# Performance work log

Measured on AMD Instinct MI355X. Metric: run time of the kernel, lower is better.

Reference implementation:

```python
import jax, jax.numpy as jnp
import numpy as np

N, E, G = 20000, 320000, 256
F = 128
C = [256, 512, 1024]
NHID, NOUT = 1024, 768
EPS = 1e-5


def setup_inputs() -> dict:
    key = jax.random.key(0)
    keys = iter(jax.random.split(key, 64))
    def nrm(shape, s=0.02):
        return jax.random.normal(next(keys), shape, jnp.float32) * s
    inp = {}
    inp["x"] = jax.random.normal(next(keys), (N, F), jnp.float32)
    inp["edge_index"] = jax.random.randint(next(keys), (2, E), 0, N)
    inp["batch"] = jnp.sort(jax.random.randint(next(keys), (N,), 0, G))
    # stem GCNConv: F -> C[0]
    inp["w0"] = nrm((F, C[0])); inp["b0"] = jnp.zeros((C[0],), jnp.float32)
    # residual blocks
    for i in range(2):
        cin, cout = C[i], C[i + 1]
        mid = cin + (cout - cin) // 2
        p = f"blk{i}_"
        inp[p + "w1"] = nrm((cin, mid)); inp[p + "b1"] = jnp.zeros((mid,), jnp.float32)
        inp[p + "g1"] = jnp.ones((mid,), jnp.float32); inp[p + "be1"] = jnp.zeros((mid,), jnp.float32)
        inp[p + "w2"] = nrm((mid, cout)); inp[p + "b2"] = jnp.zeros((cout,), jnp.float32)
        inp[p + "g2"] = jnp.ones((cout,), jnp.float32); inp[p + "be2"] = jnp.zeros((cout,), jnp.float32)
        inp[p + "w3"] = nrm((cin, cout)); inp[p + "b3"] = jnp.zeros((cout,), jnp.float32)
    inp["mw1"] = nrm((C[-1], NHID)); inp["mb1"] = jnp.zeros((NHID,), jnp.float32)
    inp["mw2"] = nrm((NHID, NOUT)); inp["mb2"] = jnp.zeros((NOUT,), jnp.float32)
    return inp


def _gcn(x, w, b, src, dst, dinv):
    # PyG GCNConv: D^{-1/2}(A+I)D^{-1/2} X W + b, deg computed with self-loops
    xw = x @ w                                     # [N, Cout]
    msg = xw[src] * dinv[src, None]                # [E, Cout]
    agg = jax.ops.segment_sum(msg, dst, num_segments=x.shape[0])
    return agg * dinv[:, None] + xw * (dinv * dinv)[:, None] + b


def _bn(h, g, b):
    # BatchNorm1d in training mode: biased batch statistics over nodes
    m = h.mean(axis=0)
    v = h.var(axis=0)
    return g * (h - m) * jax.lax.rsqrt(v + EPS) + b


def reference(x, edge_index, batch, w0, b0,
              blk0_w1, blk0_b1, blk0_g1, blk0_be1, blk0_w2, blk0_b2, blk0_g2, blk0_be2, blk0_w3, blk0_b3,
              blk1_w1, blk1_b1, blk1_g1, blk1_be1, blk1_w2, blk1_b2, blk1_g2, blk1_be2, blk1_w3, blk1_b3,
              mw1, mb1, mw2, mb2):
    src, dst = edge_index[0], edge_index[1]
    deg = 1.0 + jax.ops.segment_sum(jnp.ones((src.shape[0],), x.dtype), dst, num_segments=x.shape[0])
    dinv = jax.lax.rsqrt(deg)                      # deg >= 1, no zero guard needed

    h = jax.nn.relu(_gcn(x, w0, b0, src, dst, dinv))
    blocks = [
        (blk0_w1, blk0_b1, blk0_g1, blk0_be1, blk0_w2, blk0_b2, blk0_g2, blk0_be2, blk0_w3, blk0_b3),
        (blk1_w1, blk1_b1, blk1_g1, blk1_be1, blk1_w2, blk1_b2, blk1_g2, blk1_be2, blk1_w3, blk1_b3),
    ]
    for (w1, b1, g1, be1, w2, b2, g2, be2, w3, b3) in blocks:
        t = jax.nn.relu(_bn(_gcn(h, w1, b1, src, dst, dinv), g1, be1))
        t = jax.nn.relu(_bn(_gcn(t, w2, b2, src, dst, dinv), g2, be2))
        h = jax.nn.relu(t) + _gcn(h, w3, b3, src, dst, dinv)

    # global mean pool over graphs
    s = jax.ops.segment_sum(h, batch, num_segments=G)
    cnt = jax.ops.segment_sum(jnp.ones((h.shape[0],), h.dtype), batch, num_segments=G)
    pooled = s / jnp.maximum(cnt, 1.0)[:, None]    # [G, C[-1]]

    out = jax.nn.relu(pooled @ mw1 + mb1) @ mw2 + mb2
    return out
```

## Files before the change

### kernel.cpp

```cpp
#include <hip/hip_runtime.h>
#include <cstdint>
#include <cstddef>

#define NN 20000
#define NE 320000
#define NG 256
#define NB 79

typedef unsigned short u16;
typedef __attribute__((ext_vector_type(8))) short bf16x8;
typedef __attribute__((ext_vector_type(4))) float f32x4;

__device__ inline float b2f(u16 h){
  union { unsigned u; float f; } v; v.u = ((unsigned)h) << 16; return v.f;
}
__device__ inline u16 f2b(float f){
  union { float f; unsigned u; } v; v.f = f;
  unsigned r = v.u + 0x7FFFu + ((v.u >> 16) & 1u);
  return (u16)(r >> 16);
}
__device__ inline void up8(const uint4& v, float* a){
  union { unsigned u; float f; } t;
  t.u = v.x << 16;         a[0] = t.f;
  t.u = v.x & 0xffff0000u; a[1] = t.f;
  t.u = v.y << 16;         a[2] = t.f;
  t.u = v.y & 0xffff0000u; a[3] = t.f;
  t.u = v.z << 16;         a[4] = t.f;
  t.u = v.z & 0xffff0000u; a[5] = t.f;
  t.u = v.w << 16;         a[6] = t.f;
  t.u = v.w & 0xffff0000u; a[7] = t.f;
}
__device__ inline unsigned pk2(float a, float b){
  return (unsigned)f2b(a) | (((unsigned)f2b(b)) << 16);
}

__device__ inline void gload_lds16(const void* g, void* l){
  __builtin_amdgcn_global_load_lds(
      (const __attribute__((address_space(1))) unsigned int*)g,
      (__attribute__((address_space(3))) unsigned int*)l, 16, 0, 0);
}


__global__ void k_zero(int* __restrict__ p, int n){
  int i = blockIdx.x*blockDim.x + threadIdx.x;
  if (i < n) p[i] = 0;
}

__global__ void k_deg(const int* __restrict__ ei, int* __restrict__ deg){
  int e = blockIdx.x*blockDim.x + threadIdx.x;
  if (e < NE) atomicAdd(&deg[ei[NE + e]], 1);
}

__global__ void k_scan1(const int* __restrict__ counts, int* __restrict__ bsum,
                        float* __restrict__ dinv){
  __shared__ int sm[256];
  int b = blockIdx.x, tid = threadIdx.x, idx = b*256 + tid;
  int v = (idx < NN) ? counts[idx] : 0;
  if (idx < NN) dinv[idx] = rsqrtf(1.0f + (float)v);
  sm[tid] = v;
  __syncthreads();
  for (int d = 128; d > 0; d >>= 1){
    if (tid < d) sm[tid] += sm[tid + d];
    __syncthreads();
  }
  if (tid == 0) bsum[b] = sm[0];
}
__global__ void k_scan2(int* __restrict__ bsum){
  if (threadIdx.x == 0){
    int c = 0;
    for (int i = 0; i < NB; i++){ int t = bsum[i]; bsum[i] = c; c += t; }
    bsum[NB] = c;
  }
}
__global__ void k_scan3(const int* __restrict__ counts, const int* __restrict__ bsum,
                        int* __restrict__ offs){
  __shared__ int sm[256];
  int b = blockIdx.x, tid = threadIdx.x, idx = b*256 + tid;
  int v = (idx < NN) ? counts[idx] : 0;
  sm[tid] = v;
  __syncthreads();
  for (int d = 1; d < 256; d <<= 1){
    int t = (tid >= d) ? sm[tid - d] : 0;
    __syncthreads();
    sm[tid] += t;
    __syncthreads();
  }
  if (idx < NN) offs[idx] = bsum[b] + sm[tid] - v;
  if (idx == NN - 1) offs[NN] = bsum[NB];
}

__global__ void k_fill(const int* __restrict__ ei, const int* __restrict__ offs,
                       int* __restrict__ cur, int* __restrict__ srcs){
  int e = blockIdx.x*blockDim.x + threadIdx.x;
  if (e < NE){
    int s = ei[e];
    int d = ei[NE + e];
    int p = atomicAdd(&cur[d], 1);
    srcs[offs[d] + p] = s;
  }
}

__global__ void k_bounds(const int* __restrict__ batch, int* __restrict__ start){
  int i = blockIdx.x*blockDim.x + threadIdx.x;
  if (i < NN){
    int b  = batch[i];
    int bp = (i == 0) ? -1 : batch[i-1];
    for (int g = bp + 1; g <= b; g++) start[g] = i;
    if (i == NN - 1){
      for (int g = b + 1; g <= NG; g++) start[g] = NN;
    }
  }
}

__global__ void k_cast(const float4* __restrict__ x, ushort4* __restrict__ xb,
                       const float* __restrict__ dinv, int total4){
  int t = blockIdx.x*blockDim.x + threadIdx.x;
  if (t >= total4) return;
  float di = dinv[t >> 5];
  float4 v = x[t];
  ushort4 o; o.x = f2b(v.x * di); o.y = f2b(v.y * di);
  o.z = f2b(v.z * di); o.w = f2b(v.w * di);
  xb[t] = o;
}

struct WPArgs {
  const float* w[7];
  u16* wt[7];
  int K[7], N[7];
  int tstart[8];
};
__global__ __launch_bounds__(256) void k_wprep7(WPArgs a){
  __shared__ float sm[64][65];
  int bid = blockIdx.x;
  int wi = 0;
  while (wi < 6 && bid >= a.tstart[wi+1]) wi++;
  int tt = bid - a.tstart[wi];
  int K = a.K[wi], N = a.N[wi];
  int nk = K >> 6;
  int kb = (tt % nk) * 64, nb = (tt / nk) * 64;
  const float* w = a.w[wi];
  u16* wt = a.wt[wi];
  int tid = threadIdx.x;
  #pragma unroll
  for (int i = 0; i < 16; i++){
    int t = i*256 + tid;
    int r = t >> 6, c = t & 63;
    sm[r][c] = w[(size_t)(kb + r) * N + nb + c];
  }
  __syncthreads();
  #pragma unroll
  for (int i = 0; i < 16; i++){
    int t = i*256 + tid;
    int r = t >> 6, c = t & 63;
    wt[(size_t)(nb + r) * K + kb + c] = f2b(sm[c][r]);
  }
}

template<int C8>
__global__ __launch_bounds__(256) void k_bnscale(uint4* __restrict__ buf,
                        const float* __restrict__ dinv,
                        const float* __restrict__ sumv, const float* __restrict__ sqv,
                        const float* __restrict__ gam,  const float* __restrict__ bet){
  int t = blockIdx.x*blockDim.x + threadIdx.x;
  if (t >= NN * C8) return;
  int i = t / C8;
  int c = t - i * C8;
  float sc[8], sh[8];
  #pragma unroll
  for (int k = 0; k < 8; k++){
    int ch = c*8 + k;
    float m  = sumv[ch] * (1.0f / NN);
    float vv = sqv[ch] * (1.0f / NN) - m * m;
    float rs = rsqrtf(vv + 1e-5f);
    sc[k] = gam[ch] * rs;
    sh[k] = bet[ch] - m * sc[k];
  }
  float di = dinv[i];
  float a[8];
  up8(buf[t], a);
  #pragma unroll
  for (int k = 0; k < 8; k++) a[k] = fmaxf(fmaf(a[k], sc[k], sh[k]), 0.f) * di;
  uint4 o;
  o.x = pk2(a[0], a[1]); o.y = pk2(a[2], a[3]);
  o.z = pk2(a[4], a[5]); o.w = pk2(a[6], a[7]);
  buf[t] = o;
}

template<int C8, int C8G>
__global__ __launch_bounds__(256) void k_agg_b(const uint4* __restrict__ in, uint4* __restrict__ out,
                        const float* __restrict__ dinv, const int* __restrict__ offs,
                        const int* __restrict__ srcs){
  constexpr bool PART = (C8G != C8);
  int bid = blockIdx.x;
  int g = PART ? (bid & 7) : 0;
  int t = PART ? ((bid >> 3)*256 + threadIdx.x) : (bid*256 + threadIdx.x);
  if (t >= NN * C8G) return;
  int i = t / C8G;
  int c = g * C8G + (t - i * C8G);
  float acc[8];
  up8(in[(size_t)i * C8 + c], acc);
  int e = offs[i], e1 = offs[i + 1];
  for (; e + 4 <= e1; e += 4){
    int sA = srcs[e], sB = srcs[e+1], sC = srcs[e+2], sD = srcs[e+3];
    uint4 yA = in[(size_t)sA * C8 + c];
    uint4 yB = in[(size_t)sB * C8 + c];
    uint4 yC = in[(size_t)sC * C8 + c];
    uint4 yD = in[(size_t)sD * C8 + c];
    float b[8];
    up8(yA, b);
    #pragma unroll
    for (int k = 0; k < 8; k++) acc[k] += b[k];
    up8(yB, b);
    #pragma unroll
    for (int k = 0; k < 8; k++) acc[k] += b[k];
    up8(yC, b);
    #pragma unroll
    for (int k = 0; k < 8; k++) acc[k] += b[k];
    up8(yD, b);
    #pragma unroll
    for (int k = 0; k < 8; k++) acc[k] += b[k];
  }
  for (; e < e1; e++){
    int s = srcs[e];
    float b[8];
    up8(in[(size_t)s * C8 + c], b);
    #pragma unroll
    for (int k = 0; k < 8; k++) acc[k] += b[k];
  }
  float di = dinv[i];
  #pragma unroll
  for (int k = 0; k < 8; k++) acc[k] *= di;
  uint4 o;
  o.x = pk2(acc[0], acc[1]); o.y = pk2(acc[2], acc[3]);
  o.z = pk2(acc[4], acc[5]); o.w = pk2(acc[6], acc[7]);
  out[(size_t)i * C8 + c] = o;
}

template<int MODE, bool STATS, bool SCALE>
__global__ __launch_bounds__(256, 4) void k_mfma(const u16* __restrict__ A,
                                                 const u16* __restrict__ BT,
                                                 const float* __restrict__ bias,
                                                 u16* __restrict__ C,
                                                 float* __restrict__ p0,
                                                 float* __restrict__ p1,
                                                 const float* __restrict__ p2,
                                                 const float* __restrict__ p3,
                                                 const float* __restrict__ dv,
                                                 int M, int K, int Nc){
  __shared__ u16 S[128*128];
  u16* As = S;
  u16* Bs = S + 128*64;
  const int tid = threadIdx.x;
  const int lane = tid & 63;
  const int quad = lane >> 4;
  const int l16 = lane & 15;
  const int wid = tid >> 6;
  const int wm = wid & 1, wn = wid >> 1;

  const int nwg = gridDim.x * gridDim.y;
  const int p = blockIdx.y * gridDim.x + blockIdx.x;
  const int xcd = p & 7;
  const int q = nwg >> 3, r = nwg & 7;
  const int w = (xcd < r ? xcd * (q + 1) : r * (q + 1) + (xcd - r) * q) + (p >> 3);
  const int bn = (w % gridDim.x) * 128;
  const int bm = (w / gridDim.x) * 128;

  f32x4 acc[4][4];
  #pragma unroll
  for (int i = 0; i < 4; i++)
    #pragma unroll
    for (int j = 0; j < 4; j++)
      acc[i][j] = (f32x4){0.f, 0.f, 0.f, 0.f};

  const int srow = tid >> 3;
  const int scol8 = tid & 7;
  for (int k0 = 0; k0 < K; k0 += 64){
    #pragma unroll
    for (int i = 0; i < 4; i++){
      int row = i*32 + srow;
      int gc = (scol8 ^ (row & 7)) * 8;
      int lofs = row*64 + scol8*8;
      gload_lds16(A + (size_t)(bm + row) * K + k0 + gc, As + lofs);
      gload_lds16(BT + (size_t)(bn + row) * K + k0 + gc, Bs + lofs);
    }
    __syncthreads();
    #pragma unroll
    for (int kk = 0; kk < 2; kk++){
      const int col8 = kk*4 + quad;
      bf16x8 af[4], bfr[4];
      #pragma unroll
      for (int mi = 0; mi < 4; mi++){
        int row = wm*64 + mi*16 + l16;
        af[mi] = *(const bf16x8*)(As + row*64 + ((col8 ^ (row & 7)) * 8));
      }
      #pragma unroll
      for (int ni = 0; ni < 4; ni++){
        int row = wn*64 + ni*16 + l16;
        bfr[ni] = *(const bf16x8*)(Bs + row*64 + ((col8 ^ (row & 7)) * 8));
      }
      #pragma unroll
      for (int mi = 0; mi < 4; mi++)
        #pragma unroll
        for (int ni = 0; ni < 4; ni++)
          acc[mi][ni] = __builtin_amdgcn_mfma_f32_16x16x32_bf16(af[mi], bfr[ni], acc[mi][ni], 0, 0, 0);
    }
    __syncthreads();
  }
  #pragma unroll
  for (int ni = 0; ni < 4; ni++){
    int colL = wn*64 + ni*16 + l16;
    float bb = bias[bn + colL];
    float s = 0.f, s2 = 0.f;
    #pragma unroll
    for (int mi = 0; mi < 4; mi++){
      int rbase = wm*64 + mi*16 + quad*4;
      #pragma unroll
      for (int r2 = 0; r2 < 4; r2++){
        int rowL = rbase + r2;
        float v = acc[mi][ni][r2] + bb;
        if (STATS && (bm + rowL) < M){ s += v; s2 += v * v; }
        if (MODE == 1) v = fmaxf(v, 0.f);
        S[rowL*128 + colL] = f2b(v);
      }
    }
    if (STATS){
      s  += __shfl_xor(s, 16, 64);  s  += __shfl_xor(s, 32, 64);
      s2 += __shfl_xor(s2, 16, 64); s2 += __shfl_xor(s2, 32, 64);
      if (quad == 0){
        atomicAdd(&p0[bn + colL], s);
        atomicAdd(&p1[bn + colL], s2);
      }
    }
  }
  __syncthreads();
  #pragma unroll
  for (int it = 0; it < 8; it++){
    int idx = it*256 + tid;
    int rl = idx >> 4, cq = idx & 15;
    int row = bm + rl;
    if (row < M){
      int col0 = bn + cq*8;
      uint4 wv = *(const uint4*)(S + rl*128 + cq*8);
      u16* cp = C + (size_t)row * Nc + col0;
      if (MODE == 3){
        float di = SCALE ? dv[row] : 1.f;
        float o[8], ov[8];
        up8(wv, o);
        uint4 old = *(const uint4*)cp;
        up8(old, ov);
        #pragma unroll
        for (int k = 0; k < 8; k++){
          int ch = col0 + k;
          float m  = p0[ch] * (1.0f / NN);
          float vv = p1[ch] * (1.0f / NN) - m * m;
          float rs = rsqrtf(vv + 1e-5f);
          float sc = p2[ch] * rs;
          float sh = p3[ch] - m * sc;
          o[k] += fmaxf(fmaf(ov[k], sc, sh), 0.f);
          if (SCALE) o[k] *= di;
        }
        uint4 ou;
        ou.x = pk2(o[0], o[1]); ou.y = pk2(o[2], o[3]);
        ou.z = pk2(o[4], o[5]); ou.w = pk2(o[6], o[7]);
        *(uint4*)cp = ou;
      } else if (SCALE){
        float di = dv[row];
        float o[8];
        up8(wv, o);
        #pragma unroll
        for (int k = 0; k < 8; k++) o[k] *= di;
        uint4 ou;
        ou.x = pk2(o[0], o[1]); ou.y = pk2(o[2], o[3]);
        ou.z = pk2(o[4], o[5]); ou.w = pk2(o[6], o[7]);
        *(uint4*)cp = ou;
      } else {
        *(uint4*)cp = wv;
      }
    }
  }
}

template<bool RELUA>
__global__ __launch_bounds__(256) void k_gemm_sk(const float* __restrict__ A,
                                                 const float* __restrict__ B,
                                                 const float* __restrict__ bias,
                                                 float* __restrict__ C,
                                                 int M, int K, int Nc){
  __shared__ float As[16][68];
  __shared__ float Bs[16][64];
  const int tid = threadIdx.x;
  const int tx = tid & 15, ty = tid >> 4;
  const int bm = blockIdx.x * 64, bn = blockIdx.y * 64;
  const int kchunk = K / gridDim.z;
  const int ks = blockIdx.z * kchunk, ke = ks + kchunk;
  const int arow = tid >> 2, akq = (tid & 3) << 2;
  const int brow = tid >> 4, bcol = (tid & 15) << 2;
  float acc[4][4] = {{0.f}};
  const bool aval = (bm + arow) < M;
  const float* Aptr = A + (size_t)(bm + arow) * K + akq;
  const float* Bptr = B + (size_t)brow * Nc + bn + bcol;
  for (int k0 = ks; k0 < ke; k0 += 16){
    float4 av = make_float4(0.f, 0.f, 0.f, 0.f);
    if (aval) av = *(const float4*)(Aptr + k0);
    if (RELUA){
      av.x = fmaxf(av.x, 0.f); av.y = fmaxf(av.y, 0.f);
      av.z = fmaxf(av.z, 0.f); av.w = fmaxf(av.w, 0.f);
    }
    float4 bv = *(const float4*)(Bptr + (size_t)k0 * Nc);
    As[akq + 0][arow] = av.x;
    As[akq + 1][arow] = av.y;
    As[akq + 2][arow] = av.z;
    As[akq + 3][arow] = av.w;
    *(float4*)&Bs[brow][bcol] = bv;
    __syncthreads();
    #pragma unroll
    for (int kk = 0; kk < 16; kk++){
      const float4 a = *(const float4*)(&As[kk][ty << 2]);
      const float4 b = *(const float4*)(&Bs[kk][tx << 2]);
      const float ar[4] = {a.x, a.y, a.z, a.w};
      const float br[4] = {b.x, b.y, b.z, b.w};
      #pragma unroll
      for (int i = 0; i < 4; i++)
        #pragma unroll
        for (int j = 0; j < 4; j++)
          acc[i][j] = fmaf(ar[i], br[j], acc[i][j]);
    }
    __syncthreads();
  }
  const int col = bn + (tx << 2);
  float4 bb = make_float4(0.f, 0.f, 0.f, 0.f);
  if (blockIdx.z == 0) bb = *(const float4*)(bias + col);
  #pragma unroll
  for (int i = 0; i < 4; i++){
    int row = bm + (ty << 2) + i;
    if (row < M){
      float* cp = C + (size_t)row * Nc + col;
      atomicAdd(cp + 0, acc[i][0] + bb.x);
      atomicAdd(cp + 1, acc[i][1] + bb.y);
      atomicAdd(cp + 2, acc[i][2] + bb.z);
      atomicAdd(cp + 3, acc[i][3] + bb.w);
    }
  }
}

__global__ __launch_bounds__(256) void k_pool_b(const u16* __restrict__ h,
                                                const int* __restrict__ start,
                                                float* __restrict__ pooled){
  __shared__ float sm[128*8];
  int g = blockIdx.x;
  int half = threadIdx.x >> 7;
  int cb = threadIdx.x & 127;
  int c = cb << 3;
  int r0 = start[g], r1 = start[g + 1];
  float acc[8] = {0.f,0.f,0.f,0.f,0.f,0.f,0.f,0.f};
  for (int r = r0 + half; r < r1; r += 2){
    float b[8];
    up8(*(const uint4*)(h + (size_t)r * 1024 + c), b);
    #pragma unroll
    for (int k = 0; k < 8; k++) acc[k] += b[k];
  }
  if (half){
    #pragma unroll
    for (int k = 0; k < 8; k++) sm[cb*8 + k] = acc[k];
  }
  __syncthreads();
  if (!half){
    float inv = (r1 > r0) ? (1.0f / (float)(r1 - r0)) : 0.0f;
    float o[8];
    #pragma unroll
    for (int k = 0; k < 8; k++) o[k] = (acc[k] + sm[cb*8 + k]) * inv;
    float4* dst = (float4*)(pooled + (size_t)g * 1024 + c);
    dst[0] = make_float4(o[0], o[1], o[2], o[3]);
    dst[1] = make_float4(o[4], o[5], o[6], o[7]);
  }
}


extern "C" void kernel_launch(void* const* d_in, const int* in_sizes, int n_in,
                              void* d_out, int out_size, void* d_ws, size_t ws_size,
                              hipStream_t stream) {
  const float* x    = (const float*)d_in[0];
  const int*   ei   = (const int*)d_in[1];
  const int*   bat  = (const int*)d_in[2];
  const float* w0   = (const float*)d_in[3];
  const float* b0   = (const float*)d_in[4];
  const float* a_w1 = (const float*)d_in[5],  *a_b1  = (const float*)d_in[6];
  const float* a_g1 = (const float*)d_in[7],  *a_be1 = (const float*)d_in[8];
  const float* a_w2 = (const float*)d_in[9],  *a_b2  = (const float*)d_in[10];
  const float* a_g2 = (const float*)d_in[11], *a_be2 = (const float*)d_in[12];
  const float* a_w3 = (const float*)d_in[13], *a_b3  = (const float*)d_in[14];
  const float* c_w1 = (const float*)d_in[15], *c_b1  = (const float*)d_in[16];
  const float* c_g1 = (const float*)d_in[17], *c_be1 = (const float*)d_in[18];
  const float* c_w2 = (const float*)d_in[19], *c_b2  = (const float*)d_in[20];
  const float* c_g2 = (const float*)d_in[21], *c_be2 = (const float*)d_in[22];
  const float* c_w3 = (const float*)d_in[23], *c_b3  = (const float*)d_in[24];
  const float* mw1  = (const float*)d_in[25], *mb1   = (const float*)d_in[26];
  const float* mw2  = (const float*)d_in[27], *mb2   = (const float*)d_in[28];
  float* out = (float*)d_out;

  char* pp = (char*)d_ws;
  auto alloc = [&](size_t b)->char*{ char* r = pp; pp += (b + 255) & ~(size_t)255; return r; };

  const size_t CH = (size_t)NN * 2;
  char* R = alloc(2304 * CH);
  float* dinv = (float*)alloc((size_t)NN * 4);
  int* icomb  = (int*)alloc((size_t)2 * NN * 4);
  int* deg    = icomb;
  int* cur    = icomb + NN;
  int* offs   = (int*)alloc((size_t)(NN + 1) * 4);
  int* bsum   = (int*)alloc((size_t)(NB + 1) * 4);
  int* srcs   = (int*)alloc((size_t)NE * 4);
  int* startg = (int*)alloc((size_t)(NG + 1) * 4);
  float* SB   = (float*)alloc(5376 * 4);
  float* sA1 = SB;
  float* sA2 = SB + 768;
  float* sC1 = SB + 1792;
  float* sC2 = SB + 3328;
  u16* WT  = (u16*)alloc(2162688 * 2);
  u16* wt0  = WT;
  u16* wtA1 = WT + 32768;
  u16* wtA2 = WT + 131072;
  u16* wtA3 = WT + 327680;
  u16* wtC1 = WT + 458752;
  u16* wtC2 = WT + 851968;
  u16* wtC3 = WT + 1638400;
  float* P  = (float*)WT;
  float* Hh = P + (size_t)NG * 1024;

  auto slot = [&](int s)->u16*{ return (u16*)(R + (size_t)s * CH); };
  u16* xb  = slot(512);
  u16* ax  = slot(0);
  u16* h0  = slot(128);
  u16* ah0 = slot(1664);
  u16* t1  = slot(1920);
  u16* at  = slot(1280);
  u16* h1  = slot(768);
  u16* ah1 = slot(1792);
  u16* u1  = slot(0);
  u16* au  = slot(1024);
  u16* h2  = slot(0);

  auto cdiv = [](int a, int b){ return (a + b - 1) / b; };

  k_zero<<<cdiv(2*NN,256),256,0,stream>>>(icomb, 2*NN);
  k_zero<<<cdiv(5376,256),256,0,stream>>>((int*)SB, 5376);
  k_deg <<<cdiv(NE,256),256,0,stream>>>(ei, deg);
  k_scan1<<<NB,256,0,stream>>>(deg, bsum, dinv);
  k_scan2<<<1,64,0,stream>>>(bsum);
  k_scan3<<<NB,256,0,stream>>>(deg, bsum, offs);
  k_fill<<<cdiv(NE,256),256,0,stream>>>(ei, offs, cur, srcs);
  k_bounds<<<cdiv(NN,256),256,0,stream>>>(bat, startg);
  k_cast<<<cdiv(NN*32,256),256,0,stream>>>((const float4*)x, (ushort4*)xb, dinv, NN*32);

  {
    WPArgs wa;
    const float* ws[7] = {w0, a_w1, a_w2, a_w3, c_w1, c_w2, c_w3};
    u16* wts[7] = {wt0, wtA1, wtA2, wtA3, wtC1, wtC2, wtC3};
    int Ks[7] = {128, 256, 384, 256, 512, 768, 512};
    int Ns[7] = {256, 384, 512, 512, 768, 1024, 1024};
    int acc = 0;
    for (int i = 0; i < 7; i++){
      wa.w[i] = ws[i]; wa.wt[i] = wts[i]; wa.K[i] = Ks[i]; wa.N[i] = Ns[i];
      wa.tstart[i] = acc;
      acc += (Ks[i]/64) * (Ns[i]/64);
    }
    wa.tstart[7] = acc;
    k_wprep7<<<acc,256,0,stream>>>(wa);
  }

  auto agg = [&](const u16* in, u16* o, int C){
    int C8 = C / 8;
    switch (C8){
      case 16: k_agg_b<16,16><<<cdiv(NN*16,256),256,0,stream>>>((const uint4*)in,(uint4*)o,dinv,offs,srcs); break;
      case 32: k_agg_b<32,32><<<cdiv(NN*32,256),256,0,stream>>>((const uint4*)in,(uint4*)o,dinv,offs,srcs); break;
      case 48: k_agg_b<48, 6><<<8*cdiv(NN*6,256),256,0,stream>>>((const uint4*)in,(uint4*)o,dinv,offs,srcs); break;
      case 64: k_agg_b<64, 8><<<8*cdiv(NN*8,256),256,0,stream>>>((const uint4*)in,(uint4*)o,dinv,offs,srcs); break;
      case 96: k_agg_b<96,12><<<8*cdiv(NN*12,256),256,0,stream>>>((const uint4*)in,(uint4*)o,dinv,offs,srcs); break;
      default: break;
    }
  };
  auto gemm_m = [&](const u16* A, const u16* BT_, const float* bi, u16* Cc,
                    int K, int Nc, int mode, float* st, int sC,
                    const float* g2, const float* b2, bool scale3){
    dim3 g(Nc/128, cdiv(NN,128));
    if (mode == 0)
      k_mfma<0,true,false><<<g,256,0,stream>>>(A, BT_, bi, Cc, st, st + sC, nullptr, nullptr, dinv, NN, K, Nc);
    else if (mode == 1)
      k_mfma<1,false,true><<<g,256,0,stream>>>(A, BT_, bi, Cc, nullptr, nullptr, nullptr, nullptr, dinv, NN, K, Nc);
    else if (scale3)
      k_mfma<3,false,true><<<g,256,0,stream>>>(A, BT_, bi, Cc, st, st + sC, g2, b2, dinv, NN, K, Nc);
    else
      k_mfma<3,false,false><<<g,256,0,stream>>>(A, BT_, bi, Cc, st, st + sC, g2, b2, dinv, NN, K, Nc);
  };

  agg(xb, ax, 128);
  gemm_m(ax, wt0, b0, h0, 128, 256, 1, nullptr, 0, nullptr, nullptr, false);
  agg(h0, ah0, 256);
  gemm_m(ah0, wtA1, a_b1, t1, 256, 384, 0, sA1, 384, nullptr, nullptr, false);
  k_bnscale<48><<<cdiv(NN*48,256),256,0,stream>>>((uint4*)t1, dinv, sA1, sA1+384, a_g1, a_be1);
  agg(t1, at, 384);
  gemm_m(at, wtA2, a_b2, h1, 384, 512, 0, sA2, 512, nullptr, nullptr, false);
  gemm_m(ah0, wtA3, a_b3, h1, 256, 512, 3, sA2, 512, a_g2, a_be2, true);
  agg(h1, ah1, 512);
  gemm_m(ah1, wtC1, c_b1, u1, 512, 768, 0, sC1, 768, nullptr, nullptr, false);
  k_bnscale<96><<<cdiv(NN*96,256),256,0,stream>>>((uint4*)u1, dinv, sC1, sC1+768, c_g1, c_be1);
  agg(u1, au, 768);
  gemm_m(au, wtC2, c_b2, h2, 768, 1024, 0, sC2, 1024, nullptr, nullptr, false);
  gemm_m(ah1, wtC3, c_b3, h2, 512, 1024, 3, sC2, 1024, c_g2, c_be2, false);
  k_pool_b<<<NG,256,0,stream>>>(h2, startg, P);
  {
    k_zero<<<cdiv(NG*1024,256),256,0,stream>>>((int*)Hh, NG*1024);
    k_zero<<<cdiv(NG*768,256),256,0,stream>>>((int*)out, NG*768);
    dim3 g1(cdiv(NG,64), 1024/64, 8);
    k_gemm_sk<false><<<g1,256,0,stream>>>(P, mw1, mb1, Hh, NG, 1024, 1024);
    dim3 g2(cdiv(NG,64), 768/64, 8);
    k_gemm_sk<true><<<g2,256,0,stream>>>(Hh, mw2, mb2, out, NG, 1024, 768);
  }
}
```

Measured before the change: 627.1 us.

## Store aggregation inputs in channel-group-blocked layout for gather locality

Producers of aggregation inputs (cast, BN-scale, and the GEMM epilogues) now write features in a layout blocked by eight channel groups, so each group's data for all nodes is contiguous. The aggregation kernel always splits the work into eight channel-group passes and gathers neighbour rows from a compact per-group slab, which should improve cache hit rates during the random-neighbour gather. This costs extra buffers, because in-place updates become separate source and destination, and it needs a reworked buffer-slot assignment that risks aliasing errors.

```diff
diff --git a/kernel.cpp b/kernel.cpp
--- a/kernel.cpp
+++ b/kernel.cpp
@@ -112,15 +112,21 @@
   }
 }
 
-__global__ void k_cast(const float4* __restrict__ x, ushort4* __restrict__ xb,
-                       const float* __restrict__ dinv, int total4){
+__global__ void k_cast(const float* __restrict__ x, uint4* __restrict__ xb,
+                       const float* __restrict__ dinv, int total16){
   int t = blockIdx.x*blockDim.x + threadIdx.x;
-  if (t >= total4) return;
-  float di = dinv[t >> 5];
-  float4 v = x[t];
-  ushort4 o; o.x = f2b(v.x * di); o.y = f2b(v.y * di);
-  o.z = f2b(v.z * di); o.w = f2b(v.w * di);
-  xb[t] = o;
+  if (t >= total16) return;
+  int i = t >> 4;
+  int c = t & 15;
+  float di = dinv[i];
+  const float* xp = x + (size_t)i*128 + c*8;
+  float4 a = *(const float4*)xp;
+  float4 b = *(const float4*)(xp + 4);
+  uint4 o;
+  o.x = pk2(a.x*di, a.y*di); o.y = pk2(a.z*di, a.w*di);
+  o.z = pk2(b.x*di, b.y*di); o.w = pk2(b.z*di, b.w*di);
+  int g = c >> 1, cl = c & 1;
+  xb[(size_t)g*NN*2 + (size_t)i*2 + cl] = o;
 }
 
 struct WPArgs {
@@ -157,10 +163,12 @@
 }
 
 template<int C8>
-__global__ __launch_bounds__(256) void k_bnscale(uint4* __restrict__ buf,
+__global__ __launch_bounds__(256) void k_bnscale(const uint4* __restrict__ src,
+                        uint4* __restrict__ dst,
                         const float* __restrict__ dinv,
                         const float* __restrict__ sumv, const float* __restrict__ sqv,
                         const float* __restrict__ gam,  const float* __restrict__ bet){
+  constexpr int C8G = C8 / 8;
   int t = blockIdx.x*blockDim.x + threadIdx.x;
   if (t >= NN * C8) return;
   int i = t / C8;
@@ -177,35 +185,36 @@
   }
   float di = dinv[i];
   float a[8];
-  up8(buf[t], a);
+  up8(src[t], a);
   #pragma unroll
   for (int k = 0; k < 8; k++) a[k] = fmaxf(fmaf(a[k], sc[k], sh[k]), 0.f) * di;
   uint4 o;
   o.x = pk2(a[0], a[1]); o.y = pk2(a[2], a[3]);
   o.z = pk2(a[4], a[5]); o.w = pk2(a[6], a[7]);
-  buf[t] = o;
+  int g = c / C8G, cl = c - g * C8G;
+  dst[(size_t)g*NN*C8G + (size_t)i*C8G + cl] = o;
 }
 
 template<int C8, int C8G>
 __global__ __launch_bounds__(256) void k_agg_b(const uint4* __restrict__ in, uint4* __restrict__ out,
                         const float* __restrict__ dinv, const int* __restrict__ offs,
                         const int* __restrict__ srcs){
-  constexpr bool PART = (C8G != C8);
   int bid = blockIdx.x;
-  int g = PART ? (bid & 7) : 0;
-  int t = PART ? ((bid >> 3)*256 + threadIdx.x) : (bid*256 + threadIdx.x);
+  int g = bid & 7;
+  int t = (bid >> 3)*256 + threadIdx.x;
   if (t >= NN * C8G) return;
   int i = t / C8G;
-  int c = g * C8G + (t - i * C8G);
+  int cl = t - i * C8G;
+  const uint4* base = in + (size_t)g*NN*C8G + cl;
   float acc[8];
-  up8(in[(size_t)i * C8 + c], acc);
+  up8(base[(size_t)i * C8G], acc);
   int e = offs[i], e1 = offs[i + 1];
   for (; e + 4 <= e1; e += 4){
     int sA = srcs[e], sB = srcs[e+1], sC = srcs[e+2], sD = srcs[e+3];
-    uint4 yA = in[(size_t)sA * C8 + c];
-    uint4 yB = in[(size_t)sB * C8 + c];
-    uint4 yC = in[(size_t)sC * C8 + c];
-    uint4 yD = in[(size_t)sD * C8 + c];
+    uint4 yA = base[(size_t)sA * C8G];
+    uint4 yB = base[(size_t)sB * C8G];
+    uint4 yC = base[(size_t)sC * C8G];
+    uint4 yD = base[(size_t)sD * C8G];
     float b[8];
     up8(yA, b);
     #pragma unroll
@@ -223,7 +232,7 @@
   for (; e < e1; e++){
     int s = srcs[e];
     float b[8];
-    up8(in[(size_t)s * C8 + c], b);
+    up8(base[(size_t)s * C8G], b);
     #pragma unroll
     for (int k = 0; k < 8; k++) acc[k] += b[k];
   }
@@ -233,14 +242,15 @@
   uint4 o;
   o.x = pk2(acc[0], acc[1]); o.y = pk2(acc[2], acc[3]);
   o.z = pk2(acc[4], acc[5]); o.w = pk2(acc[6], acc[7]);
-  out[(size_t)i * C8 + c] = o;
-}
-
-template<int MODE, bool STATS, bool SCALE>
+  out[(size_t)i * C8 + g * C8G + cl] = o;
+}
+
+template<int MODE, bool STATS, bool SCALE, bool BLK>
 __global__ __launch_bounds__(256, 4) void k_mfma(const u16* __restrict__ A,
                                                  const u16* __restrict__ BT,
                                                  const float* __restrict__ bias,
-                                                 u16* __restrict__ C,
+                                                 const u16* __restrict__ C,
+                                                 u16* __restrict__ Co,
                                                  float* __restrict__ p0,
                                                  float* __restrict__ p1,
                                                  const float* __restrict__ p2,
@@ -341,12 +351,12 @@
     if (row < M){
       int col0 = bn + cq*8;
       uint4 wv = *(const uint4*)(S + rl*128 + cq*8);
-      u16* cp = C + (size_t)row * Nc + col0;
+      uint4 ou;
       if (MODE == 3){
         float di = SCALE ? dv[row] : 1.f;
         float o[8], ov[8];
         up8(wv, o);
-        uint4 old = *(const uint4*)cp;
+        uint4 old = *(const uint4*)(C + (size_t)row * Nc + col0);
         up8(old, ov);
         #pragma unroll
         for (int k = 0; k < 8; k++){
@@ -359,22 +369,27 @@
           o[k] += fmaxf(fmaf(ov[k], sc, sh), 0.f);
           if (SCALE) o[k] *= di;
         }
-        uint4 ou;
         ou.x = pk2(o[0], o[1]); ou.y = pk2(o[2], o[3]);
         ou.z = pk2(o[4], o[5]); ou.w = pk2(o[6], o[7]);
-        *(uint4*)cp = ou;
       } else if (SCALE){
         float di = dv[row];
         float o[8];
         up8(wv, o);
         #pragma unroll
         for (int k = 0; k < 8; k++) o[k] *= di;
-        uint4 ou;
         ou.x = pk2(o[0], o[1]); ou.y = pk2(o[2], o[3]);
         ou.z = pk2(o[4], o[5]); ou.w = pk2(o[6], o[7]);
-        *(uint4*)cp = ou;
       } else {
-        *(uint4*)cp = wv;
+        ou = wv;
+      }
+      if (BLK){
+        int chpg = Nc >> 3;
+        int g = col0 / chpg;
+        int c8g = chpg >> 3;
+        int cl = (col0 - g * chpg) >> 3;
+        *((uint4*)Co + (size_t)g*NN*c8g + (size_t)row*c8g + cl) = ou;
+      } else {
+        *(uint4*)(Co + (size_t)row * Nc + col0) = ou;
       }
     }
   }
@@ -528,17 +543,20 @@
   float* Hh = P + (size_t)NG * 1024;
 
   auto slot = [&](int s)->u16*{ return (u16*)(R + (size_t)s * CH); };
-  u16* xb  = slot(512);
-  u16* ax  = slot(0);
-  u16* h0  = slot(128);
-  u16* ah0 = slot(1664);
-  u16* t1  = slot(1920);
-  u16* at  = slot(1280);
-  u16* h1  = slot(768);
-  u16* ah1 = slot(1792);
-  u16* u1  = slot(0);
-  u16* au  = slot(1024);
-  u16* h2  = slot(0);
+  u16* xb    = slot(0);
+  u16* ax    = slot(128);
+  u16* h0    = slot(256);
+  u16* ah0   = slot(512);
+  u16* t1raw = slot(768);
+  u16* t1b   = slot(1152);
+  u16* at    = slot(1536);
+  u16* h1raw = slot(0);
+  u16* h1b   = slot(768);
+  u16* ah1   = slot(1792);
+  u16* u1raw = slot(0);
+  u16* u1b   = slot(768);
+  u16* au    = slot(0);
+  u16* h2    = slot(768);
 
   auto cdiv = [](int a, int b){ return (a + b - 1) / b; };
 
@@ -550,7 +568,7 @@
   k_scan3<<<NB,256,0,stream>>>(deg, bsum, offs);
   k_fill<<<cdiv(NE,256),256,0,stream>>>(ei, offs, cur, srcs);
   k_bounds<<<cdiv(NN,256),256,0,stream>>>(bat, startg);
-  k_cast<<<cdiv(NN*32,256),256,0,stream>>>((const float4*)x, (ushort4*)xb, dinv, NN*32);
+  k_cast<<<cdiv(NN*16,256),256,0,stream>>>(x, (uint4*)xb, dinv, NN*16);
 
   {
     WPArgs wa;
@@ -570,43 +588,52 @@
 
   auto agg = [&](const u16* in, u16* o, int C){
     int C8 = C / 8;
+    int C8G = C8 / 8;
+    int gb = 8 * cdiv(NN * C8G, 256);
     switch (C8){
-      case 16: k_agg_b<16,16><<<cdiv(NN*16,256),256,0,stream>>>((const uint4*)in,(uint4*)o,dinv,offs,srcs); break;
-      case 32: k_agg_b<32,32><<<cdiv(NN*32,256),256,0,stream>>>((const uint4*)in,(uint4*)o,dinv,offs,srcs); break;
-      case 48: k_agg_b<48, 6><<<8*cdiv(NN*6,256),256,0,stream>>>((const uint4*)in,(uint4*)o,dinv,offs,srcs); break;
-      case 64: k_agg_b<64, 8><<<8*cdiv(NN*8,256),256,0,stream>>>((const uint4*)in,(uint4*)o,dinv,offs,srcs); break;
-      case 96: k_agg_b<96,12><<<8*cdiv(NN*12,256),256,0,stream>>>((const uint4*)in,(uint4*)o,dinv,offs,srcs); break;
+      case 16: k_agg_b<16, 2><<<gb,256,0,stream>>>((const uint4*)in,(uint4*)o,dinv,offs,srcs); break;
+      case 32: k_agg_b<32, 4><<<gb,256,0,stream>>>((const uint4*)in,(uint4*)o,dinv,offs,srcs); break;
+      case 48: k_agg_b<48, 6><<<gb,256,0,stream>>>((const uint4*)in,(uint4*)o,dinv,offs,srcs); break;
+      case 64: k_agg_b<64, 8><<<gb,256,0,stream>>>((const uint4*)in,(uint4*)o,dinv,offs,srcs); break;
+      case 96: k_agg_b<96,12><<<gb,256,0,stream>>>((const uint4*)in,(uint4*)o,dinv,offs,srcs); break;
       default: break;
     }
   };
-  auto gemm_m = [&](const u16* A, const u16* BT_, const float* bi, u16* Cc,
-                    int K, int Nc, int mode, float* st, int sC,
-                    const float* g2, const float* b2, bool scale3){
+  auto gemm0 = [&](const u16* A, const u16* BT_, const float* bi, u16* Cc,
+                   int K, int Nc, float* st, int sC){
     dim3 g(Nc/128, cdiv(NN,128));
-    if (mode == 0)
-      k_mfma<0,true,false><<<g,256,0,stream>>>(A, BT_, bi, Cc, st, st + sC, nullptr, nullptr, dinv, NN, K, Nc);
-    else if (mode == 1)
-      k_mfma<1,false,true><<<g,256,0,stream>>>(A, BT_, bi, Cc, nullptr, nullptr, nullptr, nullptr, dinv, NN, K, Nc);
-    else if (scale3)
-      k_mfma<3,false,true><<<g,256,0,stream>>>(A, BT_, bi, Cc, st, st + sC, g2, b2, dinv, NN, K, Nc);
-    else
-      k_mfma<3,false,false><<<g,256,0,stream>>>(A, BT_, bi, Cc, st, st + sC, g2, b2, dinv, NN, K, Nc);
+    k_mfma<0,true,false,false><<<g,256,0,stream>>>(A, BT_, bi, Cc, Cc, st, st + sC, nullptr, nullptr, dinv, NN, K, Nc);
   };
+  auto gemm1b = [&](const u16* A, const u16* BT_, const float* bi, u16* Cob,
+                    int K, int Nc){
+    dim3 g(Nc/128, cdiv(NN,128));
+    k_mfma<1,false,true,true><<<g,256,0,stream>>>(A, BT_, bi, Cob, Cob, nullptr, nullptr, nullptr, nullptr, dinv, NN, K, Nc);
+  };
+  auto gemm3b = [&](const u16* A, const u16* BT_, const float* bi, const u16* Cold, u16* Cob,
+                    int K, int Nc, float* st, int sC, const float* g2, const float* b2){
+    dim3 g(Nc/128, cdiv(NN,128));
+    k_mfma<3,false,true,true><<<g,256,0,stream>>>(A, BT_, bi, Cold, Cob, st, st + sC, g2, b2, dinv, NN, K, Nc);
+  };
+  auto gemm3 = [&](const u16* A, const u16* BT_, const float* bi, u16* Cc,
+                   int K, int Nc, float* st, int sC, const float* g2, const float* b2){
+    dim3 g(Nc/128, cdiv(NN,128));
+    k_mfma<3,false,false,false><<<g,256,0,stream>>>(A, BT_, bi, Cc, Cc, st, st + sC, g2, b2, dinv, NN, K, Nc);
+  };
 
   agg(xb, ax, 128);
-  gemm_m(ax, wt0, b0, h0, 128, 256, 1, nullptr, 0, nullptr, nullptr, false);
+  gemm1b(ax, wt0, b0, h0, 128, 256);
   agg(h0, ah0, 256);
-  gemm_m(ah0, wtA1, a_b1, t1, 256, 384, 0, sA1, 384, nullptr, nullptr, false);
-  k_bnscale<48><<<cdiv(NN*48,256),256,0,stream>>>((uint4*)t1, dinv, sA1, sA1+384, a_g1, a_be1);
-  agg(t1, at, 384);
-  gemm_m(at, wtA2, a_b2, h1, 384, 512, 0, sA2, 512, nullptr, nullptr, false);
-  gemm_m(ah0, wtA3, a_b3, h1, 256, 512, 3, sA2, 512, a_g2, a_be2, true);
-  agg(h1, ah1, 512);
-  gemm_m(ah1, wtC1, c_b1, u1, 512, 768, 0, sC1, 768, nullptr, nullptr, false);
-  k_bnscale<96><<<cdiv(NN*96,256),256,0,stream>>>((uint4*)u1, dinv, sC1, sC1+768, c_g1, c_be1);
-  agg(u1, au, 768);
-  gemm_m(au, wtC2, c_b2, h2, 768, 1024, 0, sC2, 1024, nullptr, nullptr, false);
-  gemm_m(ah1, wtC3, c_b3, h2, 512, 1024, 3, sC2, 1024, c_g2, c_be2, false);
+  gemm0(ah0, wtA1, a_b1, t1raw, 256, 384, sA1, 384);
+  k_bnscale<48><<<cdiv(NN*48,256),256,0,stream>>>((const uint4*)t1raw, (uint4*)t1b, dinv, sA1, sA1+384, a_g1, a_be1);
+  agg(t1b, at, 384);
+  gemm0(at, wtA2, a_b2, h1raw, 384, 512, sA2, 512);
+  gemm3b(ah0, wtA3, a_b3, h1raw, h1b, 256, 512, sA2, 512, a_g2, a_be2);
+  agg(h1b, ah1, 512);
+  gemm0(ah1, wtC1, c_b1, u1raw, 512, 768, sC1, 768);
+  k_bnscale<96><<<cdiv(NN*96,256),256,0,stream>>>((const uint4*)u1raw, (uint4*)u1b, dinv, sC1, sC1+768, c_g1, c_be1);
+  agg(u1b, au, 768);
+  gemm0(au, wtC2, c_b2, h2, 768, 1024, sC2, 1024);
+  gemm3(ah1, wtC3, c_b3, h2, 512, 1024, sC2, 1024, c_g2, c_be2);
   k_pool_b<<<NG,256,0,stream>>>(h2, startg, P);
   {
     k_zero<<<cdiv(NG*1024,256),256,0,stream>>>((int*)Hh, NG*1024);
```

Measured after the change: 604.2 us. 1.04x faster.
